# Optimization experiments

Measured on AMD Instinct MI355X. Metric: run time of the kernel, lower is better.

The kernel has to match this reference:

```python
import jax, jax.numpy as jnp
import numpy as np

N_NODES = 50000
IN_CH = 128
OUT_CH = 64
HID = 2 * OUT_CH  # 128
N_EDGES = 800000


def _glorot(key, shape):
    fan_in, fan_out = shape[0], shape[-1]
    lim = jnp.sqrt(6.0 / (fan_in + fan_out))
    return jax.random.uniform(key, shape, jnp.float32, -lim, lim)


def setup_inputs() -> dict:
    key = jax.random.key(0)
    ks = jax.random.split(key, 10)
    x = jax.random.normal(ks[0], (N_NODES, IN_CH), jnp.float32)
    edge_index = jax.random.randint(ks[1], (2, N_EDGES), 0, N_NODES, jnp.int32)
    return {
        "x": x,
        "edge_index": edge_index,
        "W1": _glorot(ks[2], (IN_CH, HID)),
        "a_src1": _glorot(ks[3], (HID,)),
        "a_dst1": _glorot(ks[4], (HID,)),
        "b1": jnp.zeros((HID,), jnp.float32),
        "W2": _glorot(ks[5], (HID, OUT_CH)),
        "a_src2": _glorot(ks[6], (OUT_CH,)),
        "a_dst2": _glorot(ks[7], (OUT_CH,)),
        "b2": jnp.zeros((OUT_CH,), jnp.float32),
    }


def _gat_conv(x, src, dst, W, a_src, a_dst, b, n_nodes):
    # Linear transform: [N, F_out]
    h = x @ W
    # Per-node attention halves (heads=1): alpha_i = <h_i, a>
    al_s = h @ a_src  # [N]
    al_d = h @ a_dst  # [N]
    # Edge scores with LeakyReLU(0.2), PyG default negative slope
    e = jax.nn.leaky_relu(al_s[src] + al_d[dst], negative_slope=0.2)
    # Segment softmax over incoming edges of each dst node
    m = jax.ops.segment_max(e, dst, num_segments=n_nodes)
    m = jnp.where(jnp.isfinite(m), m, 0.0)
    ex = jnp.exp(e - m[dst])
    denom = jax.ops.segment_sum(ex, dst, num_segments=n_nodes)
    alpha = ex / (denom[dst] + 1e-16)  # [E]
    # Weighted scatter-add aggregation
    out = jax.ops.segment_sum(h[src] * alpha[:, None], dst, num_segments=n_nodes)
    return out + b


def reference(x, edge_index, W1, a_src1, a_dst1, b1, W2, a_src2, a_dst2, b2):
    n = x.shape[0]
    # add_self_loops=True (PyG GATConv default)
    loops = jnp.arange(n, dtype=edge_index.dtype)
    src = jnp.concatenate([edge_index[0], loops])
    dst = jnp.concatenate([edge_index[1], loops])
    h = _gat_conv(x.astype(jnp.float32), src, dst, W1, a_src1, a_dst1, b1, n)
    h = jax.nn.relu(h)
    return _gat_conv(h, src, dst, W2, a_src2, a_dst2, b2, n)
```

## Files before the change

kernel.cpp:

```cpp
#include <hip/hip_runtime.h>
#include <hip/hip_bf16.h>

#define N_NODES 50000
#define IN_CH 128
#define HID 128
#define OUT_CH 64
#define N_EDGES 800000
#define N_TOT_EDGES (N_EDGES + N_NODES)
#define ET_PAD (N_TOT_EDGES + 3 * N_NODES)
#define MPAD 50048
#define NBN ((N_NODES + 255) / 256)
#define NB_ET ((N_TOT_EDGES + 255) / 256)
#define NB_GEMM (MPAD / 64)
#define NSH 128
#define EPS (N_EDGES / NSH)
#define NDW (N_NODES / 4)

typedef float float4v __attribute__((ext_vector_type(4)));
typedef unsigned uint4v __attribute__((ext_vector_type(4)));
typedef __attribute__((ext_vector_type(8))) short bf16x8;
typedef __attribute__((ext_vector_type(4))) float f32x4;

__device__ __forceinline__ unsigned bf16_rne(float f) {
    unsigned u = __float_as_uint(f);
    return (u + 0x7fffu + ((u >> 16) & 1u)) >> 16;
}
__device__ __forceinline__ unsigned pack2(float a, float b) {
    return bf16_rne(a) | (bf16_rne(b) << 16);
}

__global__ __launch_bounds__(256) void k_pre(
        const float* __restrict__ W1, unsigned short* __restrict__ Wl1,
        const float* __restrict__ W2, unsigned short* __restrict__ Wl2) {
    const int b = blockIdx.x, t = threadIdx.x;
    const float* W; unsigned short* Wl; int N, bb;
    if (b < 8) { W = W1; Wl = Wl1; N = 128; bb = b; }
    else       { W = W2; Wl = Wl2; N = 64;  bb = b - 8; }
    const int tg = bb * 256 + t;
    if (tg >= 16 * N) return;
    const int kg = tg / N, col = tg & (N - 1);
    float v[8];
    #pragma unroll
    for (int j = 0; j < 8; ++j) v[j] = W[(size_t)(kg * 8 + j) * N + col];
    uint4 p;
    p.x = pack2(v[0], v[1]); p.y = pack2(v[2], v[3]);
    p.z = pack2(v[4], v[5]); p.w = pack2(v[6], v[7]);
    *(uint4*)&Wl[(size_t)tg * 8] = p;
}

template<int N, bool AF32, bool USELDS>
__device__ __forceinline__ void gemm_body(int gb, int t,
        const float* __restrict__ Xf, const unsigned short* __restrict__ Xb,
        const unsigned short* __restrict__ Wlg,
        const float* __restrict__ asrc, const float* __restrict__ adst,
        unsigned short* __restrict__ Hb, float* __restrict__ als,
        float* __restrict__ ald, int M, unsigned short* Wl) {
    constexpr int NF = N / 16;
    const unsigned short* Wsrc;
    if constexpr (USELDS) {
        for (int i = t; i < N * 16; i += 256)
            ((uint4*)Wl)[i] = ((const uint4*)Wlg)[i];
        __syncthreads();
        Wsrc = Wl;
    } else {
        Wsrc = Wlg;
    }

    const int lane = t & 63, w = t >> 6;
    const int rb = gb * 64 + w * 16;
    const int cl = lane & 15, g = lane >> 4;

    f32x4 acc[NF];
    #pragma unroll
    for (int n = 0; n < NF; ++n) acc[n] = (f32x4){0.f, 0.f, 0.f, 0.f};

    const float* Xrow = nullptr;
    const unsigned short* Abase = nullptr;
    if constexpr (AF32) {
        const int arow = (rb + cl < M) ? (rb + cl) : (M - 1);
        Xrow = Xf + (size_t)arow * 128;
    } else {
        Abase = Xb + (size_t)(rb >> 4) * 2048 + cl * 8;
    }

    #pragma unroll
    for (int s = 0; s < 4; ++s) {
        bf16x8 af;
        if constexpr (AF32) {
            const int k0 = (s * 4 + g) * 8;
            float4 a = *(const float4*)&Xrow[k0];
            float4 c = *(const float4*)&Xrow[k0 + 4];
            uint4v uu;
            uu[0] = pack2(a.x, a.y); uu[1] = pack2(a.z, a.w);
            uu[2] = pack2(c.x, c.y); uu[3] = pack2(c.z, c.w);
            af = __builtin_bit_cast(bf16x8, uu);
        } else {
            af = *(const bf16x8*)(Abase + (s * 4 + g) * 128);
        }
        #pragma unroll
        for (int n = 0; n < NF; ++n) {
            bf16x8 bf = *(const bf16x8*)(Wsrc + ((s * 4 + g) * N + n * 16 + cl) * 8);
            acc[n] = __builtin_amdgcn_mfma_f32_16x16x32_bf16(af, bf, acc[n], 0, 0, 0);
        }
    }

    float asv[NF], adv[NF];
    #pragma unroll
    for (int n = 0; n < NF; ++n) {
        asv[n] = asrc[n * 16 + cl];
        adv[n] = adst[n * 16 + cl];
    }

    #pragma unroll
    for (int r = 0; r < 4; ++r) {
        float ps = 0.f, pd = 0.f;
        #pragma unroll
        for (int n = 0; n < NF; ++n) {
            ps += acc[n][r] * asv[n];
            pd += acc[n][r] * adv[n];
        }
        #pragma unroll
        for (int mask = 1; mask < 16; mask <<= 1) {
            ps += __shfl_xor(ps, mask);
            pd += __shfl_xor(pd, mask);
        }
        const int row = rb + g * 4 + r;
        if (cl == 0 && row < M) { als[row] = ps; ald[row] = pd; }
    }

    #pragma unroll
    for (int r = 0; r < 4; ++r) {
        const int row = rb + g * 4 + r;
        if (row >= M) continue;
        #pragma unroll
        for (int n = 0; n < NF; ++n)
            Hb[(size_t)(n >> 1) * (size_t)M * 32 + (size_t)row * 32
               + (n & 1) * 16 + cl] = (unsigned short)bf16_rne(acc[n][r]);
    }
}

__global__ __launch_bounds__(256) void k_par1(
        const int* __restrict__ ei, unsigned* __restrict__ cnt_s,
        unsigned char* __restrict__ rank8,
        const float* __restrict__ X, const unsigned short* __restrict__ Wl1,
        const float* __restrict__ asrc, const float* __restrict__ adst,
        unsigned short* __restrict__ Hb, float* __restrict__ als,
        float* __restrict__ ald, int M) {
    __shared__ unsigned lcnt[NDW];
    const int b = blockIdx.x, t = threadIdx.x;
    if (b < NSH) {
        const int s = b;
        for (int i = t; i < NDW; i += 256) lcnt[i] = 0;
        __syncthreads();
        const int base = s * EPS;
        const int* __restrict__ dst = ei + N_EDGES;
        for (int j = base + t; j < base + EPS; j += 256) {
            int d = __builtin_nontemporal_load(&dst[j]);
            unsigned sh = 8u * (d & 3);
            unsigned old = atomicAdd(&lcnt[d >> 2], 1u << sh);
            rank8[j] = (unsigned char)((old >> sh) & 0xFFu);
        }
        __syncthreads();
        unsigned* __restrict__ outp = cnt_s + (size_t)s * NDW;
        for (int i = t; i < NDW; i += 256) outp[i] = lcnt[i];
        return;
    }
    gemm_body<HID, true, false>(b - NSH, t, X, nullptr, Wl1,
                                asrc, adst, Hb, als, ald, M, nullptr);
}

__global__ void k_scan1(const unsigned* __restrict__ cnt_s, int* __restrict__ cntT,
                        unsigned char* __restrict__ pcoff8,
                        int* __restrict__ off, int* __restrict__ bsum, int n) {
    __shared__ int s[256];
    int t = threadIdx.x;
    int i = blockIdx.x * 256 + t;
    int padded = 0;
    if (i < n) {
        const int dw = i >> 2;
        const unsigned sh = 8u * (i & 3);
        int pc = 1;
        for (int c = 0; c < NSH; ++c) {
            pcoff8[(size_t)c * n + i] = (unsigned char)pc;
            pc += (int)((cnt_s[(size_t)c * NDW + dw] >> sh) & 0xFFu);
        }
        cntT[i] = pc;
        padded = (pc + 3) & ~3;
    }
    s[t] = padded;
    __syncthreads();
    for (int d = 1; d < 256; d <<= 1) {
        int x = (t >= d) ? s[t - d] : 0;
        __syncthreads();
        s[t] += x;
        __syncthreads();
    }
    if (i < n) off[i + 1] = s[t];
    if (t == 255) bsum[blockIdx.x] = s[255];
}

__global__ void k_scan3(int* __restrict__ off, const int* __restrict__ bsum, int n) {
    __shared__ int s[256];
    int t = threadIdx.x;
    s[t] = (t < NBN) ? bsum[t] : 0;
    __syncthreads();
    for (int d = 1; d < 256; d <<= 1) {
        int x = (t >= d) ? s[t - d] : 0;
        __syncthreads();
        s[t] += x;
        __syncthreads();
    }
    int base = (blockIdx.x > 0) ? s[blockIdx.x - 1] : 0;
    int i = blockIdx.x * 256 + t;
    if (i < n) off[i + 1] += base;
    if (i == 0) off[0] = 0;
}

__global__ void k_fillw(const int* __restrict__ ei, const int* __restrict__ off,
                        const unsigned char* __restrict__ rank8,
                        const unsigned char* __restrict__ pcoff8,
                        const float* __restrict__ als, const float* __restrict__ ald,
                        unsigned* __restrict__ ew, int e, int n) {
    int i = blockIdx.x * 256 + threadIdx.x;
    if (i < e) {
        int src = __builtin_nontemporal_load(&ei[i]);
        int dst = __builtin_nontemporal_load(&ei[e + i]);
        int c = i / EPS;
        int pos = off[dst] + (int)pcoff8[(size_t)c * n + dst] + (int)rank8[i];
        float ev = als[src] + ald[dst];
        ev = ev > 0.f ? ev : 0.2f * ev;
        ew[pos] = ((unsigned)src << 16) | bf16_rne(__expf(ev));
    } else if (i < e + n) {
        int v = i - e;
        float ev = als[v] + ald[v];
        ev = ev > 0.f ? ev : 0.2f * ev;
        ew[off[v]] = ((unsigned)v << 16) | bf16_rne(__expf(ev));
    }
}

__global__ __launch_bounds__(256) void gemm_mfma64(
        const unsigned short* __restrict__ Xb, const unsigned short* __restrict__ Wlg,
        const float* __restrict__ asrc, const float* __restrict__ adst,
        unsigned short* __restrict__ Hb, float* __restrict__ als,
        float* __restrict__ ald, int M) {
    __shared__ unsigned short Wl[16 * 64 * 8];
    gemm_body<OUT_CH, false, true>(blockIdx.x, threadIdx.x, nullptr, Xb, Wlg,
                                   asrc, adst, Hb, als, ald, M, Wl);
}

template<int F, bool RELU, bool PACKOUT, bool INLINEW>
__global__ __launch_bounds__(256) void k_spmm_b(
        const unsigned short* __restrict__ Hb, const unsigned* __restrict__ ew,
        const float* __restrict__ als, const float* __restrict__ ald,
        const float* __restrict__ bias, const int* __restrict__ off,
        const int* __restrict__ cntT, void* __restrict__ outv, int n) {
    constexpr int NCH = F / 32;
    const int chunk = blockIdx.x % NCH;
    const int v = (blockIdx.x / NCH) * 64 + (threadIdx.x >> 2);
    if (v >= n) return;
    const int q = threadIdx.x & 3;
    const int start = off[v], pend = off[v + 1];
    const int rend = start + cntT[v];
    const float aldv = INLINEW ? ald[v] : 0.f;
    const unsigned short* __restrict__ Hch = Hb + (size_t)chunk * (size_t)n * 32 + q * 8;

    float a0[8] = {}, a1[8] = {}, a2[8] = {}, a3[8] = {};
    float denom = 0.f;

    #define GATB(E, A, IDX)                                              \
        {                                                                \
            float w_;                                                    \
            if (INLINEW) {                                               \
                int s_ = (int)((E) >> 16);                               \
                float e_ = als[s_] + aldv;                               \
                e_ = e_ > 0.f ? e_ : 0.2f * e_;                          \
                w_ = __expf(e_);                                         \
            } else {                                                     \
                w_ = __uint_as_float((E) << 16);                         \
            }                                                            \
            w_ = ((IDX) < rend) ? w_ : 0.f;                              \
            denom += w_;                                                 \
            uint4 h_ = *(const uint4*)&Hch[(size_t)((E) >> 16) * 32];    \
            A[0] += w_ * __uint_as_float(h_.x << 16);                    \
            A[1] += w_ * __uint_as_float(h_.x & 0xffff0000u);            \
            A[2] += w_ * __uint_as_float(h_.y << 16);                    \
            A[3] += w_ * __uint_as_float(h_.y & 0xffff0000u);            \
            A[4] += w_ * __uint_as_float(h_.z << 16);                    \
            A[5] += w_ * __uint_as_float(h_.z & 0xffff0000u);            \
            A[6] += w_ * __uint_as_float(h_.w << 16);                    \
            A[7] += w_ * __uint_as_float(h_.w & 0xffff0000u);            \
        }
    #define GATB4(Q, J) GATB((Q).x, a0, (J)) GATB((Q).y, a1, (J)+1) \
                        GATB((Q).z, a2, (J)+2) GATB((Q).w, a3, (J)+3)

    int j = start;
    for (; j + 4 < pend; j += 8) {
        uint4 eA = *(const uint4*)&ew[j];
        uint4 eB = *(const uint4*)&ew[j + 4];
        GATB4(eA, j)
        GATB4(eB, j + 4)
    }
    if (j < pend) {
        uint4 eA = *(const uint4*)&ew[j];
        GATB4(eA, j)
    }
    #undef GATB4
    #undef GATB

    const float inv = 1.f / (denom + 1e-16f);
    const float* __restrict__ bp = bias + chunk * 32 + q * 8;
    float s[8];
    #pragma unroll
    for (int i = 0; i < 8; ++i) {
        s[i] = (a0[i] + a1[i] + a2[i] + a3[i]) * inv + bp[i];
        if (RELU) s[i] = fmaxf(s[i], 0.f);
    }

    if (PACKOUT) {
        unsigned short* Xb2 = (unsigned short*)outv;
        const int kg = chunk * 4 + q;
        uint4v p;
        p[0] = pack2(s[0], s[1]); p[1] = pack2(s[2], s[3]);
        p[2] = pack2(s[4], s[5]); p[3] = pack2(s[6], s[7]);
        __builtin_nontemporal_store(p,
            (uint4v*)&Xb2[(size_t)(v >> 4) * 2048 + kg * 128 + (v & 15) * 8]);
    } else {
        float* out = (float*)outv;
        float4v o0, o1;
        o0[0] = s[0]; o0[1] = s[1]; o0[2] = s[2]; o0[3] = s[3];
        o1[0] = s[4]; o1[1] = s[5]; o1[2] = s[6]; o1[3] = s[7];
        float* op = out + (size_t)v * F + chunk * 32 + q * 8;
        __builtin_nontemporal_store(o0, (float4v*)op);
        __builtin_nontemporal_store(o1, (float4v*)(op + 4));
    }
}


extern "C" void kernel_launch(void* const* d_in, const int* in_sizes, int n_in,
                              void* d_out, int out_size, void* d_ws, size_t ws_size,
                              hipStream_t stream) {
    const float* x     = (const float*)d_in[0];
    const int*   ei    = (const int*)d_in[1];
    const float* W1    = (const float*)d_in[2];
    const float* as1   = (const float*)d_in[3];
    const float* ad1   = (const float*)d_in[4];
    const float* b1    = (const float*)d_in[5];
    const float* W2    = (const float*)d_in[6];
    const float* as2   = (const float*)d_in[7];
    const float* ad2   = (const float*)d_in[8];
    const float* b2    = (const float*)d_in[9];
    float* out = (float*)d_out;

    const int Nn = N_NODES;

    char* ws = (char*)d_ws;
    size_t o = 0;
    auto carve = [&](size_t bytes) { char* p = ws + o; o = (o + bytes + 255) & ~(size_t)255; return p; };
    int*            off   = (int*)carve((Nn + 1) * sizeof(int));
    int*            cntT  = (int*)carve(Nn * sizeof(int));
    int*            bsum  = (int*)carve(256 * sizeof(int));
    unsigned char*  rank8 = (unsigned char*)carve((size_t)N_EDGES);
    unsigned*       cnt_s = (unsigned*)carve((size_t)NSH * NDW * sizeof(unsigned));
    unsigned char*  pcoff8= (unsigned char*)carve((size_t)NSH * Nn);
    unsigned*       ew    = (unsigned*)carve((size_t)ET_PAD * sizeof(unsigned));
    unsigned short* h1b   = (unsigned short*)carve((size_t)Nn * HID * sizeof(unsigned short));
    unsigned short* h2b   = (unsigned short*)carve((size_t)Nn * OUT_CH * sizeof(unsigned short));
    unsigned short* Xb2   = (unsigned short*)carve((size_t)MPAD * 128 * sizeof(unsigned short));
    unsigned short* Wl1   = (unsigned short*)carve(16 * 128 * 8 * sizeof(unsigned short));
    unsigned short* Wl2   = (unsigned short*)carve(16 * 64 * 8 * sizeof(unsigned short));
    float*          als1v = (float*)carve(Nn * sizeof(float));
    float*          ald1v = (float*)carve(Nn * sizeof(float));
    float*          als2v = (float*)carve(Nn * sizeof(float));
    float*          ald2v = (float*)carve(Nn * sizeof(float));

    k_pre<<<12, 256, 0, stream>>>(W1, Wl1, W2, Wl2);

    k_par1<<<NSH + NB_GEMM, 256, 0, stream>>>(
        ei, cnt_s, rank8, x, Wl1, as1, ad1, h1b, als1v, ald1v, Nn);

    k_scan1<<<NBN, 256, 0, stream>>>(cnt_s, cntT, pcoff8, off, bsum, Nn);
    k_scan3<<<NBN, 256, 0, stream>>>(off, bsum, Nn);

    k_fillw<<<NB_ET, 256, 0, stream>>>(ei, off, rank8, pcoff8, als1v, ald1v,
                                       ew, N_EDGES, Nn);

    const int nbN64 = (Nn + 63) / 64;

    k_spmm_b<HID, true, true, false><<<nbN64 * (HID / 32), 256, 0, stream>>>(
        h1b, ew, nullptr, nullptr, b1, off, cntT, Xb2, Nn);

    gemm_mfma64<<<NB_GEMM, 256, 0, stream>>>(
        Xb2, Wl2, as2, ad2, h2b, als2v, ald2v, Nn);

    k_spmm_b<OUT_CH, false, false, true><<<nbN64 * (OUT_CH / 32), 256, 0, stream>>>(
        h2b, ew, als2v, ald2v, b2, off, cntT, out, Nn);
}
```

Before: 142.2 us.

## Cut kernel launches by fusing weight prep and scan passes with a ticket

Removes the separate weight-preconversion kernel: layer-1 weights are read as fp32 and converted to bf16 inside the GEMM, and layer-2 weight packing runs on extra blocks of the scan kernel. The second scan pass is folded into the first through a last-block ticket, which computes per-block prefix bases (P2). Consumers then add that base when they read offsets, so the fix-up pass over the offset array goes away. Together this drops two launches and one pass over the offsets, at the cost of strided fp32 weight loads and repeated conversion in every GEMM block, plus an extra P2 read on each offset lookup.

```diff
diff --git a/kernel.cpp b/kernel.cpp
--- a/kernel.cpp
+++ b/kernel.cpp
@@ -29,41 +29,26 @@
     return bf16_rne(a) | (bf16_rne(b) << 16);
 }
 
-__global__ __launch_bounds__(256) void k_pre(
-        const float* __restrict__ W1, unsigned short* __restrict__ Wl1,
-        const float* __restrict__ W2, unsigned short* __restrict__ Wl2) {
-    const int b = blockIdx.x, t = threadIdx.x;
-    const float* W; unsigned short* Wl; int N, bb;
-    if (b < 8) { W = W1; Wl = Wl1; N = 128; bb = b; }
-    else       { W = W2; Wl = Wl2; N = 64;  bb = b - 8; }
-    const int tg = bb * 256 + t;
-    if (tg >= 16 * N) return;
-    const int kg = tg / N, col = tg & (N - 1);
-    float v[8];
-    #pragma unroll
-    for (int j = 0; j < 8; ++j) v[j] = W[(size_t)(kg * 8 + j) * N + col];
-    uint4 p;
-    p.x = pack2(v[0], v[1]); p.y = pack2(v[2], v[3]);
-    p.z = pack2(v[4], v[5]); p.w = pack2(v[6], v[7]);
-    *(uint4*)&Wl[(size_t)tg * 8] = p;
-}
-
-template<int N, bool AF32, bool USELDS>
+template<int N, bool AF32, bool WF32, bool USELDS>
 __device__ __forceinline__ void gemm_body(int gb, int t,
         const float* __restrict__ Xf, const unsigned short* __restrict__ Xb,
-        const unsigned short* __restrict__ Wlg,
+        const void* __restrict__ Wsrc0,
         const float* __restrict__ asrc, const float* __restrict__ adst,
         unsigned short* __restrict__ Hb, float* __restrict__ als,
         float* __restrict__ ald, int M, unsigned short* Wl) {
     constexpr int NF = N / 16;
-    const unsigned short* Wsrc;
-    if constexpr (USELDS) {
+    const unsigned short* Wsrc = nullptr;
+    const float* Wf = nullptr;
+    if constexpr (WF32) {
+        Wf = (const float*)Wsrc0;
+    } else if constexpr (USELDS) {
+        const unsigned short* Wlg = (const unsigned short*)Wsrc0;
         for (int i = t; i < N * 16; i += 256)
             ((uint4*)Wl)[i] = ((const uint4*)Wlg)[i];
         __syncthreads();
         Wsrc = Wl;
     } else {
-        Wsrc = Wlg;
+        Wsrc = (const unsigned short*)Wsrc0;
     }
 
     const int lane = t & 63, w = t >> 6;
@@ -99,8 +84,20 @@
         }
         #pragma unroll
         for (int n = 0; n < NF; ++n) {
-            bf16x8 bf = *(const bf16x8*)(Wsrc + ((s * 4 + g) * N + n * 16 + cl) * 8);
-            acc[n] = __builtin_amdgcn_mfma_f32_16x16x32_bf16(af, bf, acc[n], 0, 0, 0);
+            bf16x8 bfv;
+            if constexpr (WF32) {
+                const int k0 = (s * 4 + g) * 8, col = n * 16 + cl;
+                float wv[8];
+                #pragma unroll
+                for (int j = 0; j < 8; ++j) wv[j] = Wf[(size_t)(k0 + j) * N + col];
+                uint4v uu;
+                uu[0] = pack2(wv[0], wv[1]); uu[1] = pack2(wv[2], wv[3]);
+                uu[2] = pack2(wv[4], wv[5]); uu[3] = pack2(wv[6], wv[7]);
+                bfv = __builtin_bit_cast(bf16x8, uu);
+            } else {
+                bfv = *(const bf16x8*)(Wsrc + ((s * 4 + g) * N + n * 16 + cl) * 8);
+            }
+            acc[n] = __builtin_amdgcn_mfma_f32_16x16x32_bf16(af, bfv, acc[n], 0, 0, 0);
         }
     }
 
@@ -142,12 +139,13 @@
 __global__ __launch_bounds__(256) void k_par1(
         const int* __restrict__ ei, unsigned* __restrict__ cnt_s,
         unsigned char* __restrict__ rank8,
-        const float* __restrict__ X, const unsigned short* __restrict__ Wl1,
+        const float* __restrict__ X, const float* __restrict__ W1,
         const float* __restrict__ asrc, const float* __restrict__ adst,
         unsigned short* __restrict__ Hb, float* __restrict__ als,
-        float* __restrict__ ald, int M) {
+        float* __restrict__ ald, int* __restrict__ ticket, int M) {
     __shared__ unsigned lcnt[NDW];
     const int b = blockIdx.x, t = threadIdx.x;
+    if (b == 0 && t == 0) *ticket = 0;
     if (b < NSH) {
         const int s = b;
         for (int i = t; i < NDW; i += 256) lcnt[i] = 0;
@@ -165,16 +163,33 @@
         for (int i = t; i < NDW; i += 256) outp[i] = lcnt[i];
         return;
     }
-    gemm_body<HID, true, false>(b - NSH, t, X, nullptr, Wl1,
-                                asrc, adst, Hb, als, ald, M, nullptr);
+    gemm_body<HID, true, true, false>(b - NSH, t, X, nullptr, W1,
+                                      asrc, adst, Hb, als, ald, M, nullptr);
 }
 
 __global__ void k_scan1(const unsigned* __restrict__ cnt_s, int* __restrict__ cntT,
                         unsigned char* __restrict__ pcoff8,
-                        int* __restrict__ off, int* __restrict__ bsum, int n) {
+                        int* __restrict__ off, int* __restrict__ bsum,
+                        int* __restrict__ ticket, int* __restrict__ P2,
+                        const float* __restrict__ W2, unsigned short* __restrict__ Wl2,
+                        int n) {
     __shared__ int s[256];
-    int t = threadIdx.x;
-    int i = blockIdx.x * 256 + t;
+    __shared__ int isLast;
+    const int b = blockIdx.x, t = threadIdx.x;
+    if (b >= NBN) {
+        const int tg = (b - NBN) * 256 + t;
+        if (tg >= 16 * 64) return;
+        const int kg = tg >> 6, col = tg & 63;
+        float v[8];
+        #pragma unroll
+        for (int j = 0; j < 8; ++j) v[j] = W2[(size_t)(kg * 8 + j) * 64 + col];
+        uint4 p;
+        p.x = pack2(v[0], v[1]); p.y = pack2(v[2], v[3]);
+        p.z = pack2(v[4], v[5]); p.w = pack2(v[6], v[7]);
+        *(uint4*)&Wl2[(size_t)tg * 8] = p;
+        return;
+    }
+    int i = b * 256 + t;
     int padded = 0;
     if (i < n) {
         const int dw = i >> 2;
@@ -196,13 +211,15 @@
         __syncthreads();
     }
     if (i < n) off[i + 1] = s[t];
-    if (t == 255) bsum[blockIdx.x] = s[255];
-}
-
-__global__ void k_scan3(int* __restrict__ off, const int* __restrict__ bsum, int n) {
-    __shared__ int s[256];
-    int t = threadIdx.x;
-    s[t] = (t < NBN) ? bsum[t] : 0;
+    if (i == 0) off[0] = 0;
+    if (t == 255) bsum[b] = s[255];
+    __threadfence();
+    if (t == 0) isLast = (atomicAdd(ticket, 1) == NBN - 1);
+    __syncthreads();
+    if (!isLast) return;
+    __threadfence();
+    int v = (t < NBN) ? bsum[t] : 0;
+    s[t] = v;
     __syncthreads();
     for (int d = 1; d < 256; d <<= 1) {
         int x = (t >= d) ? s[t - d] : 0;
@@ -210,13 +227,15 @@
         s[t] += x;
         __syncthreads();
     }
-    int base = (blockIdx.x > 0) ? s[blockIdx.x - 1] : 0;
-    int i = blockIdx.x * 256 + t;
-    if (i < n) off[i + 1] += base;
-    if (i == 0) off[0] = 0;
+    if (t < NBN) P2[t] = s[t] - v;
+}
+
+__device__ __forceinline__ int off_base(const int* __restrict__ P2, int j) {
+    return (j > 0) ? P2[(j - 1) >> 8] : 0;
 }
 
 __global__ void k_fillw(const int* __restrict__ ei, const int* __restrict__ off,
+                        const int* __restrict__ P2,
                         const unsigned char* __restrict__ rank8,
                         const unsigned char* __restrict__ pcoff8,
                         const float* __restrict__ als, const float* __restrict__ ald,
@@ -226,7 +245,8 @@
         int src = __builtin_nontemporal_load(&ei[i]);
         int dst = __builtin_nontemporal_load(&ei[e + i]);
         int c = i / EPS;
-        int pos = off[dst] + (int)pcoff8[(size_t)c * n + dst] + (int)rank8[i];
+        int pos = off[dst] + off_base(P2, dst)
+                + (int)pcoff8[(size_t)c * n + dst] + (int)rank8[i];
         float ev = als[src] + ald[dst];
         ev = ev > 0.f ? ev : 0.2f * ev;
         ew[pos] = ((unsigned)src << 16) | bf16_rne(__expf(ev));
@@ -234,7 +254,7 @@
         int v = i - e;
         float ev = als[v] + ald[v];
         ev = ev > 0.f ? ev : 0.2f * ev;
-        ew[off[v]] = ((unsigned)v << 16) | bf16_rne(__expf(ev));
+        ew[off[v] + off_base(P2, v)] = ((unsigned)v << 16) | bf16_rne(__expf(ev));
     }
 }
 
@@ -244,8 +264,8 @@
         unsigned short* __restrict__ Hb, float* __restrict__ als,
         float* __restrict__ ald, int M) {
     __shared__ unsigned short Wl[16 * 64 * 8];
-    gemm_body<OUT_CH, false, true>(blockIdx.x, threadIdx.x, nullptr, Xb, Wlg,
-                                   asrc, adst, Hb, als, ald, M, Wl);
+    gemm_body<OUT_CH, false, false, true>(blockIdx.x, threadIdx.x, nullptr, Xb, Wlg,
+                                          asrc, adst, Hb, als, ald, M, Wl);
 }
 
 template<int F, bool RELU, bool PACKOUT, bool INLINEW>
@@ -253,14 +273,16 @@
         const unsigned short* __restrict__ Hb, const unsigned* __restrict__ ew,
         const float* __restrict__ als, const float* __restrict__ ald,
         const float* __restrict__ bias, const int* __restrict__ off,
-        const int* __restrict__ cntT, void* __restrict__ outv, int n) {
+        const int* __restrict__ P2, const int* __restrict__ cntT,
+        void* __restrict__ outv, int n) {
     constexpr int NCH = F / 32;
     const int chunk = blockIdx.x % NCH;
     const int v = (blockIdx.x / NCH) * 64 + (threadIdx.x >> 2);
     if (v >= n) return;
     const int q = threadIdx.x & 3;
-    const int start = off[v], pend = off[v + 1];
-    const int rend = start + cntT[v];
+    const int start = off[v] + off_base(P2, v);
+    const int pend  = off[v + 1] + P2[v >> 8];
+    const int rend  = start + cntT[v];
     const float aldv = INLINEW ? ald[v] : 0.f;
     const unsigned short* __restrict__ Hch = Hb + (size_t)chunk * (size_t)n * 32 + q * 8;
 
@@ -359,6 +381,8 @@
     int*            off   = (int*)carve((Nn + 1) * sizeof(int));
     int*            cntT  = (int*)carve(Nn * sizeof(int));
     int*            bsum  = (int*)carve(256 * sizeof(int));
+    int*            ticket= (int*)carve(256);
+    int*            P2    = (int*)carve(256 * sizeof(int));
     unsigned char*  rank8 = (unsigned char*)carve((size_t)N_EDGES);
     unsigned*       cnt_s = (unsigned*)carve((size_t)NSH * NDW * sizeof(unsigned));
     unsigned char*  pcoff8= (unsigned char*)carve((size_t)NSH * Nn);
@@ -366,32 +390,29 @@
     unsigned short* h1b   = (unsigned short*)carve((size_t)Nn * HID * sizeof(unsigned short));
     unsigned short* h2b   = (unsigned short*)carve((size_t)Nn * OUT_CH * sizeof(unsigned short));
     unsigned short* Xb2   = (unsigned short*)carve((size_t)MPAD * 128 * sizeof(unsigned short));
-    unsigned short* Wl1   = (unsigned short*)carve(16 * 128 * 8 * sizeof(unsigned short));
     unsigned short* Wl2   = (unsigned short*)carve(16 * 64 * 8 * sizeof(unsigned short));
     float*          als1v = (float*)carve(Nn * sizeof(float));
     float*          ald1v = (float*)carve(Nn * sizeof(float));
     float*          als2v = (float*)carve(Nn * sizeof(float));
     float*          ald2v = (float*)carve(Nn * sizeof(float));
 
-    k_pre<<<12, 256, 0, stream>>>(W1, Wl1, W2, Wl2);
-
     k_par1<<<NSH + NB_GEMM, 256, 0, stream>>>(
-        ei, cnt_s, rank8, x, Wl1, as1, ad1, h1b, als1v, ald1v, Nn);
-
-    k_scan1<<<NBN, 256, 0, stream>>>(cnt_s, cntT, pcoff8, off, bsum, Nn);
-    k_scan3<<<NBN, 256, 0, stream>>>(off, bsum, Nn);
-
-    k_fillw<<<NB_ET, 256, 0, stream>>>(ei, off, rank8, pcoff8, als1v, ald1v,
-                                       ew, N_EDGES, Nn);
+        ei, cnt_s, rank8, x, W1, as1, ad1, h1b, als1v, ald1v, ticket, Nn);
+
+    k_scan1<<<NBN + 4, 256, 0, stream>>>(
+        cnt_s, cntT, pcoff8, off, bsum, ticket, P2, W2, Wl2, Nn);
+
+    k_fillw<<<NB_ET, 256, 0, stream>>>(ei, off, P2, rank8, pcoff8,
+                                       als1v, ald1v, ew, N_EDGES, Nn);
 
     const int nbN64 = (Nn + 63) / 64;
 
     k_spmm_b<HID, true, true, false><<<nbN64 * (HID / 32), 256, 0, stream>>>(
-        h1b, ew, nullptr, nullptr, b1, off, cntT, Xb2, Nn);
+        h1b, ew, nullptr, nullptr, b1, off, P2, cntT, Xb2, Nn);
 
     gemm_mfma64<<<NB_GEMM, 256, 0, stream>>>(
         Xb2, Wl2, as2, ad2, h2b, als2v, ald2v, Nn);
 
     k_spmm_b<OUT_CH, false, false, true><<<nbN64 * (OUT_CH / 32), 256, 0, stream>>>(
-        h2b, ew, als2v, ald2v, b2, off, cntT, out, Nn);
-}
+        h2b, ew, als2v, ald2v, b2, off, P2, cntT, out, Nn);
+}
```

Result: slower. 153.0 us (+7.6%).
